# Kernel optimization log

Measured on AMD Instinct MI355X. Metric: run time of the kernel, lower is better.

## Reference

```python
import jax, jax.numpy as jnp
import numpy as np

DIM = 1024
HEADS = 16
DIM_HEAD = 64
INNER = HEADS * DIM_HEAD  # 1024
SCALE = DIM_HEAD ** -0.5


def setup_inputs() -> dict:
    key = jax.random.key(0)
    k1, k2, k3, k4 = jax.random.split(key, 4)
    x = jax.random.normal(k1, (2, 2048, DIM), dtype=jnp.float32)
    # nn.Linear(dim, inner*3, bias=False): weight [3*inner, dim]; store transposed [dim, 3*inner]
    w_qkv = jax.random.normal(k2, (DIM, 3 * INNER), dtype=jnp.float32) * (DIM ** -0.5)
    w_out = jax.random.normal(k3, (INNER, DIM), dtype=jnp.float32) * (INNER ** -0.5)
    b_out = jax.random.normal(k4, (DIM,), dtype=jnp.float32) * 0.02
    return {"x": x, "w_qkv": w_qkv, "w_out": w_out, "b_out": b_out}


def _attention(x, w_qkv, w_out, b_out):
    b, n, _ = x.shape
    qkv = x @ w_qkv  # [b, n, 3*inner]
    q_chunk = qkv[..., :INNER]  # NOTE: source bug — q, k, v all come from chunk 0
    def split_heads(t):
        return t.reshape(b, n, HEADS, DIM_HEAD).transpose(0, 2, 1, 3)  # b h n d
    q = split_heads(q_chunk) * SCALE
    k = split_heads(q_chunk)
    v = split_heads(q_chunk)
    dots = jnp.einsum('bhid,bhjd->bhij', q, k)
    mask_value = -jnp.finfo(dots.dtype).max
    causal_mask = jnp.triu(jnp.ones((n, n), dtype=bool), k=1)
    dots = jnp.where(causal_mask, mask_value, dots)
    attn = jax.nn.softmax(dots, axis=-1)
    out = jnp.einsum('bhij,bhjd->bhid', attn, v)
    out = out.transpose(0, 2, 1, 3).reshape(b, n, INNER)
    return out @ w_out + b_out


def reference(x, w_qkv, w_out, b_out):
    return _attention(x, w_qkv, w_out, b_out)
```

## Files before the change

### kernel.cpp

```cpp
#include <hip/hip_runtime.h>
#include <hip/hip_bf16.h>

typedef __attribute__((ext_vector_type(8))) short short8;
typedef __attribute__((ext_vector_type(4))) short bf16x4;
typedef __attribute__((ext_vector_type(4))) float floatx4;

#define MFMA16(a, b, c) __builtin_amdgcn_mfma_f32_16x16x32_bf16((a), (b), (c), 0, 0, 0)

#if defined(__HIP_DEVICE_COMPILE__)
  #if __has_builtin(__builtin_amdgcn_mfma_f32_16x16x16bf16_1k)
    #define MFMA_PV(a, b, c) __builtin_amdgcn_mfma_f32_16x16x16bf16_1k((a), (b), (c), 0, 0, 0)
  #elif __has_builtin(__builtin_amdgcn_mfma_f32_16x16x16_bf16)
    #define MFMA_PV(a, b, c) __builtin_amdgcn_mfma_f32_16x16x16_bf16((a), (b), (c), 0, 0, 0)
  #else
    #error "no 16x16x16 bf16 MFMA builtin found on device pass"
  #endif
#else
  #define MFMA_PV(a, b, c) (c)
#endif

#define SEQ    2048
#define DIMM   1024
#define HEADS  16
#define DHEAD  64
#define ROWS   4096
#define K1 0.18033688011112043f
#define K2 (-34.62468098133512f)

__global__ void cvt_bf16_kernel(const float* __restrict__ src,
                                __hip_bfloat16* __restrict__ dst) {
    const size_t i = (size_t)(blockIdx.x * 256 + threadIdx.x) * 4;
    floatx4 v = *(const floatx4*)(src + i);
    union { bf16x4 s; __hip_bfloat16 h[4]; } u;
#pragma unroll
    for (int j = 0; j < 4; j++) u.h[j] = __float2bfloat16(v[j]);
    *(bf16x4*)(dst + i) = u.s;
}

__global__ __launch_bounds__(256) void transpose_cvt_kernel(
    const float* __restrict__ W, __hip_bfloat16* __restrict__ WT, int ld) {
    __shared__ __hip_bfloat16 tile[64][72];
    const int tid = threadIdx.x;
    const int r = tid >> 2, c0 = (tid & 3) * 16;
    const int k0 = blockIdx.x * 64;
    const int n0 = blockIdx.y * 64;
    const float* src = W + (size_t)(k0 + r) * ld + n0 + c0;
    union { short8 v; __hip_bfloat16 h[8]; } a0, a1;
#pragma unroll
    for (int j = 0; j < 8; j++) {
        a0.h[j] = __float2bfloat16(src[j]);
        a1.h[j] = __float2bfloat16(src[8 + j]);
    }
    *(short8*)&tile[r][c0]     = a0.v;
    *(short8*)&tile[r][c0 + 8] = a1.v;
    __syncthreads();
    union { short8 v; __hip_bfloat16 h[8]; } u0, u1;
#pragma unroll
    for (int j = 0; j < 8; j++) {
        u0.h[j] = tile[c0 + j][r];
        u1.h[j] = tile[c0 + 8 + j][r];
    }
    __hip_bfloat16* dst = WT + (size_t)(n0 + r) * 1024 + k0 + c0;
    *(short8*)dst       = u0.v;
    *(short8*)(dst + 8) = u1.v;
}

__global__ __launch_bounds__(256) void transpose_t_kernel(
    const __hip_bfloat16* __restrict__ t,
    __hip_bfloat16* __restrict__ Tt) {
    __shared__ __hip_bfloat16 tile[64][72];
    const int tid = threadIdx.x;
    const int r = tid >> 2, c0 = (tid & 3) * 16;
    const int row0 = blockIdx.x * 64;
    const int col0 = blockIdx.y * 64;
    const __hip_bfloat16* src = t + (size_t)(row0 + r) * DIMM + col0 + c0;
    *(short8*)&tile[r][c0]     = *(const short8*)src;
    *(short8*)&tile[r][c0 + 8] = *(const short8*)(src + 8);
    __syncthreads();
    union { short8 v; __hip_bfloat16 h[8]; } u0, u1;
#pragma unroll
    for (int j = 0; j < 8; j++) {
        u0.h[j] = tile[c0 + j][r];
        u1.h[j] = tile[c0 + 8 + j][r];
    }
    __hip_bfloat16* dst = Tt + (size_t)(col0 + r) * ROWS + row0 + c0;
    *(short8*)dst       = u0.v;
    *(short8*)(dst + 8) = u1.v;
}

template <typename CT>
__global__ __launch_bounds__(256) void gemm_bf_kernel(
    const __hip_bfloat16* __restrict__ A,
    const __hip_bfloat16* __restrict__ BT,
    const float* __restrict__ bias,
    CT* __restrict__ C, int M, int N, int K) {
    __shared__ __align__(16) __hip_bfloat16 As[2][64][68];
    __shared__ __align__(16) __hip_bfloat16 Bs[2][64][68];

    const int tid  = threadIdx.x;
    const int lane = tid & 63, wid = tid >> 6;
    const int wm   = wid >> 1, wn = wid & 1;
    const int quad = lane >> 4, l15 = lane & 15;
    const int bm = blockIdx.y * 64, bn = blockIdx.x * 64;

    floatx4 acc[2][2];
#pragma unroll
    for (int r = 0; r < 2; r++)
#pragma unroll
        for (int c = 0; c < 2; c++) acc[r][c] = (floatx4){0.f, 0.f, 0.f, 0.f};

    const int sr = tid >> 2, sc = (tid & 3) * 16;
    short8 ra[2], rb[2];
    auto load_tile = [&](int k0) {
        const __hip_bfloat16* pa = A + (size_t)(bm + sr) * K + k0 + sc;
        ra[0] = *(const short8*)pa; ra[1] = *(const short8*)(pa + 8);
        const __hip_bfloat16* pb = BT + (size_t)(bn + sr) * K + k0 + sc;
        rb[0] = *(const short8*)pb; rb[1] = *(const short8*)(pb + 8);
    };
    auto store_tile = [&](int buf) {
        *(short8*)&As[buf][sr][sc]     = ra[0];
        *(short8*)&As[buf][sr][sc + 8] = ra[1];
        *(short8*)&Bs[buf][sr][sc]     = rb[0];
        *(short8*)&Bs[buf][sr][sc + 8] = rb[1];
    };

    load_tile(0);
    store_tile(0);
    if (K > 64) load_tile(64);
    __syncthreads();

    const int nk = K >> 6;
    for (int kb = 0; kb < nk; ++kb) {
        const int buf = kb & 1;
#pragma unroll
        for (int ks = 0; ks < 2; ks++) {
            short8 af[2], bf[2];
#pragma unroll
            for (int r = 0; r < 2; r++)
                af[r] = *(const short8*)&As[buf][wm * 32 + r * 16 + l15][ks * 32 + quad * 8];
#pragma unroll
            for (int c = 0; c < 2; c++)
                bf[c] = *(const short8*)&Bs[buf][wn * 32 + c * 16 + l15][ks * 32 + quad * 8];
#pragma unroll
            for (int r = 0; r < 2; r++)
#pragma unroll
                for (int c = 0; c < 2; c++)
                    acc[r][c] = MFMA16(af[r], bf[c], acc[r][c]);
        }
        if (kb + 1 < nk) store_tile(buf ^ 1);
        if (kb + 2 < nk) load_tile((kb + 2) << 6);
        __syncthreads();
    }

#pragma unroll
    for (int c = 0; c < 2; c++) {
        const int col = bn + wn * 32 + c * 16 + l15;
        const float bv = bias ? bias[col] : 0.f;
#pragma unroll
        for (int r = 0; r < 2; r++) {
            const int row0 = bm + wm * 32 + r * 16 + quad * 4;
#pragma unroll
            for (int i = 0; i < 4; i++) {
                const float v = acc[r][c][i] + bv;
                if constexpr (__is_same(CT, float))
                    C[(size_t)(row0 + i) * N + col] = v;
                else
                    C[(size_t)(row0 + i) * N + col] = __float2bfloat16(v);
            }
        }
    }
}

template <typename AT, typename CT>
__global__ __launch_bounds__(256) void gemm_fp_kernel(
    const AT* __restrict__ A, const float* __restrict__ B,
    const float* __restrict__ bias, CT* __restrict__ C,
    int M, int N, int K, int ldb) {
    __shared__ __align__(16) __hip_bfloat16 As[2][64][40];
    __shared__ __align__(16) __hip_bfloat16 Bs[2][128][40];
    const int tid = threadIdx.x;
    const int lane = tid & 63, wid = tid >> 6;
    const int wm = wid >> 1, wn = wid & 1;
    const int quad = lane >> 4, l15 = lane & 15;
    const int bm = blockIdx.y * 64, bn = blockIdx.x * 128;
    floatx4 acc[2][4];
#pragma unroll
    for (int r = 0; r < 2; r++)
#pragma unroll
        for (int c = 0; c < 4; c++) acc[r][c] = (floatx4){0.f, 0.f, 0.f, 0.f};
    const int a_lr = tid >> 2, a_lc = (tid & 3) * 8;
    const int b_kr = tid & 31, b_nc = (tid >> 5) * 16;
    floatx4 raf0, raf1; short8 rab; floatx4 rb[4];
    auto load_tile = [&](int k0) {
        const AT* pa = A + (size_t)(bm + a_lr) * K + k0 + a_lc;
        if constexpr (__is_same(AT, float)) {
            raf0 = *(const floatx4*)pa; raf1 = *(const floatx4*)(pa + 4);
        } else { rab = *(const short8*)pa; }
        const float* pb = B + (size_t)(k0 + b_kr) * ldb + bn + b_nc;
#pragma unroll
        for (int q = 0; q < 4; q++) rb[q] = *(const floatx4*)(pb + 4 * q);
    };
    auto store_tile = [&](int buf) {
        if constexpr (__is_same(AT, float)) {
            __align__(16) __hip_bfloat16 hh[8];
#pragma unroll
            for (int j = 0; j < 4; j++) {
                hh[j] = __float2bfloat16(raf0[j]); hh[4 + j] = __float2bfloat16(raf1[j]);
            }
            *(short8*)&As[buf][a_lr][a_lc] = *(short8*)&hh[0];
        } else { *(short8*)&As[buf][a_lr][a_lc] = rab; }
#pragma unroll
        for (int q = 0; q < 4; q++)
#pragma unroll
            for (int j = 0; j < 4; j++)
                Bs[buf][b_nc + 4 * q + j][b_kr] = __float2bfloat16(rb[q][j]);
    };
    load_tile(0); store_tile(0);
    if (K > 32) load_tile(32);
    __syncthreads();
    const int nk = K >> 5;
    for (int kb = 0; kb < nk; ++kb) {
        const int buf = kb & 1;
        short8 af[2], bf[4];
#pragma unroll
        for (int r = 0; r < 2; r++)
            af[r] = *(const short8*)&As[buf][wm * 32 + r * 16 + l15][quad * 8];
#pragma unroll
        for (int c = 0; c < 4; c++)
            bf[c] = *(const short8*)&Bs[buf][wn * 64 + c * 16 + l15][quad * 8];
#pragma unroll
        for (int r = 0; r < 2; r++)
#pragma unroll
            for (int c = 0; c < 4; c++)
                acc[r][c] = MFMA16(af[r], bf[c], acc[r][c]);
        if (kb + 1 < nk) store_tile(buf ^ 1);
        if (kb + 2 < nk) load_tile((kb + 2) << 5);
        __syncthreads();
    }
#pragma unroll
    for (int c = 0; c < 4; c++) {
        const int col = bn + wn * 64 + c * 16 + l15;
        const float bv = bias ? bias[col] : 0.f;
#pragma unroll
        for (int r = 0; r < 2; r++) {
            const int row0 = bm + wm * 32 + r * 16 + quad * 4;
#pragma unroll
            for (int i = 0; i < 4; i++) {
                const float v = acc[r][c][i] + bv;
                if constexpr (__is_same(CT, float)) C[(size_t)(row0 + i) * N + col] = v;
                else C[(size_t)(row0 + i) * N + col] = __float2bfloat16(v);
            }
        }
    }
}

__global__ __launch_bounds__(256) void attn_kernel(
    const __hip_bfloat16* __restrict__ T,
    const __hip_bfloat16* __restrict__ Tt,
    __hip_bfloat16* __restrict__ O) {
    __shared__ __align__(16) __hip_bfloat16 Ks[2][64][68];
    __shared__ __align__(16) __hip_bfloat16 Vt[2][64][68];

    const int tid  = threadIdx.x;
    const int lane = tid & 63, wid = tid >> 6;
    const int quad = lane >> 4, l15 = lane & 15;

    const int bx = blockIdx.x;
    const int half = bx >> 9, idx = bx & 511;
    const int g = idx & 15, h = (idx >> 4) & 15, b = idx >> 8;
    const int qt = half ? g : 31 - g;

    const size_t rowbase = (size_t)b * SEQ;
    const int hoff  = h * DHEAD;
    const int qrow0 = qt * 64;

    short8 qf[2];
    {
        const __hip_bfloat16* qp =
            T + (rowbase + qrow0 + wid * 16 + l15) * DIMM + hoff + quad * 8;
        qf[0] = *(const short8*)qp;
        qf[1] = *(const short8*)(qp + 32);
    }

    float l_lane = 0.f;
    floatx4 accO[4];
#pragma unroll
    for (int dt = 0; dt < 4; dt++) accO[dt] = (floatx4){0.f,0.f,0.f,0.f};

    const int sr = tid >> 2;
    const int sc = (tid & 3) * 16;

    short8 rK0, rK1, rV0, rV1;
    auto load_tile = [&](int kt) {
        const __hip_bfloat16* pK = T + (rowbase + kt * 64 + sr) * DIMM + hoff + sc;
        rK0 = *(const short8*)pK; rK1 = *(const short8*)(pK + 8);
        const __hip_bfloat16* pV =
            Tt + (size_t)(hoff + sr) * ROWS + rowbase + kt * 64 + sc;
        rV0 = *(const short8*)pV; rV1 = *(const short8*)(pV + 8);
    };
    auto store_tile = [&](int buf) {
        *(short8*)&Ks[buf][sr][sc]     = rK0;
        *(short8*)&Ks[buf][sr][sc + 8] = rK1;
        *(short8*)&Vt[buf][sr][sc]     = rV0;
        *(short8*)&Vt[buf][sr][sc + 8] = rV1;
    };

    const int last = qt;
    load_tile(0);
    store_tile(0);
    if (last >= 1) load_tile(1);
    __syncthreads();

    for (int kt = 0; kt <= last; ++kt) {
        const int buf = kt & 1;

        floatx4 s[4];
#pragma unroll
        for (int c = 0; c < 4; c++) {
            s[c] = (floatx4){0.f,0.f,0.f,0.f};
#pragma unroll
            for (int ks = 0; ks < 2; ks++) {
                short8 kfr = *(const short8*)&Ks[buf][c * 16 + l15][ks * 32 + quad * 8];
                s[c] = MFMA16(kfr, qf[ks], s[c]);
            }
        }

        bf16x4 pk[4];
        const bool need_mask = (kt == last);
#pragma unroll
        for (int c = 0; c < 4; c++) {
            union { bf16x4 v; __hip_bfloat16 hh[4]; } u;
            float sum = 0.f;
#pragma unroll
            for (int i = 0; i < 4; i++) {
                float v = exp2f(fmaf(s[c][i], K1, K2));
                if (need_mask) {
                    const int key  = kt * 64 + c * 16 + quad * 4 + i;
                    const int qrow = qrow0 + wid * 16 + l15;
                    if (key > qrow) v = 0.f;
                }
                sum += v;
                u.hh[i] = __float2bfloat16(v);
            }
            l_lane += sum;
            pk[c] = u.v;
        }

#pragma unroll
        for (int c = 0; c < 4; c++)
#pragma unroll
            for (int dt = 0; dt < 4; dt++) {
                bf16x4 vb = *(const bf16x4*)&Vt[buf][dt * 16 + l15][c * 16 + quad * 4];
                accO[dt] = MFMA_PV(pk[c], vb, accO[dt]);
            }

        if (kt < last)      store_tile(buf ^ 1);
        if (kt + 2 <= last) load_tile(kt + 2);
        __syncthreads();
    }

    l_lane += __shfl_xor(l_lane, 16);
    l_lane += __shfl_xor(l_lane, 32);
    float inv[4];
#pragma unroll
    for (int i = 0; i < 4; i++)
        inv[i] = 1.f / __shfl(l_lane, quad * 4 + i, 64);
#pragma unroll
    for (int dt = 0; dt < 4; dt++)
#pragma unroll
        for (int i = 0; i < 4; i++) {
            const size_t row = rowbase + qrow0 + wid * 16 + quad * 4 + i;
            O[row * DIMM + hoff + dt * 16 + l15] =
                __float2bfloat16(accO[dt][i] * inv[i]);
        }
}

extern "C" void kernel_launch(void* const* d_in, const int* in_sizes, int n_in,
                              void* d_out, int out_size, void* d_ws, size_t ws_size,
                              hipStream_t stream) {
    const float* x     = (const float*)d_in[0];
    const float* w_qkv = (const float*)d_in[1];
    const float* w_out = (const float*)d_in[2];
    const float* b_out = (const float*)d_in[3];
    float* out = (float*)d_out;

    __hip_bfloat16* t  = (__hip_bfloat16*)d_out;
    __hip_bfloat16* Tt = (__hip_bfloat16*)((char*)d_out + (8u << 20));
    char* ws = (char*)d_ws;
    __hip_bfloat16* ob = (__hip_bfloat16*)ws;

    if (ws_size >= (size_t)(20u << 20)) {
        __hip_bfloat16* xb  = (__hip_bfloat16*)(ws + (8u  << 20));
        __hip_bfloat16* w1t = (__hip_bfloat16*)(ws + (16u << 20));
        __hip_bfloat16* w2t = (__hip_bfloat16*)(ws + (18u << 20));

        cvt_bf16_kernel<<<4096, 256, 0, stream>>>(x, xb);
        transpose_cvt_kernel<<<dim3(16, 16), 256, 0, stream>>>(w_qkv, w1t, 3 * DIMM);
        transpose_cvt_kernel<<<dim3(16, 16), 256, 0, stream>>>(w_out, w2t, DIMM);

        gemm_bf_kernel<__hip_bfloat16><<<dim3(16, 64), 256, 0, stream>>>(
            xb, w1t, nullptr, t, ROWS, DIMM, DIMM);
        transpose_t_kernel<<<dim3(64, 16), 256, 0, stream>>>(t, Tt);
        attn_kernel<<<dim3(1024), 256, 0, stream>>>(t, Tt, ob);
        gemm_bf_kernel<float><<<dim3(16, 64), 256, 0, stream>>>(
            ob, w2t, b_out, out, ROWS, DIMM, DIMM);
    } else {
        gemm_fp_kernel<float, __hip_bfloat16><<<dim3(8, 64), 256, 0, stream>>>(
            x, w_qkv, nullptr, t, ROWS, DIMM, DIMM, 3 * DIMM);
        transpose_t_kernel<<<dim3(64, 16), 256, 0, stream>>>(t, Tt);
        attn_kernel<<<dim3(1024), 256, 0, stream>>>(t, Tt, ob);
        gemm_fp_kernel<__hip_bfloat16, float><<<dim3(8, 64), 256, 0, stream>>>(
            ob, w_out, b_out, out, ROWS, DIMM, DIMM, DIMM);
    }
}
```

Measured before the change: 167.5 us.

## Use direct global-to-LDS loads with XOR swizzle and 64x128 GEMM tiles

Rewrites the bf16 GEMM's staging so global tiles go straight into LDS via global_load_lds, skipping the register round trip and the separate store phase. The LDS layout becomes an unpadded K=32 tile with an XOR swizzle to avoid bank conflicts. The block tile widens from 64x64 to 64x128 so each wave computes 2x4 MFMA tiles, and launch bounds now request two blocks per CU. The risks are more K iterations (and syncs) per block, half as many blocks in the grid, and correctness depending on how global_load_lds places each lane's 16 bytes in LDS.

```diff
diff --git a/kernel.cpp b/kernel.cpp
--- a/kernel.cpp
+++ b/kernel.cpp
@@ -18,6 +18,13 @@
 #else
   #define MFMA_PV(a, b, c) (c)
 #endif
+
+__device__ __forceinline__ void gload16(const void* g, void* l) {
+    __builtin_amdgcn_global_load_lds(
+        (const __attribute__((address_space(1))) unsigned int*)g,
+        (__attribute__((address_space(3))) unsigned int*)l,
+        16, 0, 0);
+}
 
 #define SEQ    2048
 #define DIMM   1024
@@ -89,72 +96,77 @@
 }
 
 template <typename CT>
-__global__ __launch_bounds__(256) void gemm_bf_kernel(
+__global__ __launch_bounds__(256, 2) void gemm_bf_kernel(
     const __hip_bfloat16* __restrict__ A,
     const __hip_bfloat16* __restrict__ BT,
     const float* __restrict__ bias,
     CT* __restrict__ C, int M, int N, int K) {
-    __shared__ __align__(16) __hip_bfloat16 As[2][64][68];
-    __shared__ __align__(16) __hip_bfloat16 Bs[2][64][68];
+    __shared__ __align__(16) __hip_bfloat16 As[2][64 * 32];
+    __shared__ __align__(16) __hip_bfloat16 Bs[2][128 * 32];
 
     const int tid  = threadIdx.x;
     const int lane = tid & 63, wid = tid >> 6;
     const int wm   = wid >> 1, wn = wid & 1;
     const int quad = lane >> 4, l15 = lane & 15;
-    const int bm = blockIdx.y * 64, bn = blockIdx.x * 64;
-
-    floatx4 acc[2][2];
+    const int bm = blockIdx.y * 64, bn = blockIdx.x * 128;
+
+    floatx4 acc[2][4];
 #pragma unroll
     for (int r = 0; r < 2; r++)
 #pragma unroll
-        for (int c = 0; c < 2; c++) acc[r][c] = (floatx4){0.f, 0.f, 0.f, 0.f};
-
-    const int sr = tid >> 2, sc = (tid & 3) * 16;
-    short8 ra[2], rb[2];
-    auto load_tile = [&](int k0) {
-        const __hip_bfloat16* pa = A + (size_t)(bm + sr) * K + k0 + sc;
-        ra[0] = *(const short8*)pa; ra[1] = *(const short8*)(pa + 8);
-        const __hip_bfloat16* pb = BT + (size_t)(bn + sr) * K + k0 + sc;
-        rb[0] = *(const short8*)pb; rb[1] = *(const short8*)(pb + 8);
-    };
-    auto store_tile = [&](int buf) {
-        *(short8*)&As[buf][sr][sc]     = ra[0];
-        *(short8*)&As[buf][sr][sc + 8] = ra[1];
-        *(short8*)&Bs[buf][sr][sc]     = rb[0];
-        *(short8*)&Bs[buf][sr][sc + 8] = rb[1];
-    };
-
-    load_tile(0);
-    store_tile(0);
-    if (K > 64) load_tile(64);
+        for (int c = 0; c < 4; c++) acc[r][c] = (floatx4){0.f, 0.f, 0.f, 0.f};
+
+    const int a_r = tid >> 2;
+    const int a_c = (tid & 3) ^ ((a_r >> 1) & 3);
+    auto issueA = [&](int k0, int buf) {
+        gload16(A + (size_t)(bm + a_r) * K + k0 + a_c * 8,
+                (char*)&As[buf][0] + wid * 1024);
+    };
+    auto issueB = [&](int k0, int buf) {
+#pragma unroll
+        for (int j = 0; j < 2; j++) {
+            const int s = j * 256 + tid;
+            const int r = s >> 2;
+            const int c = (s & 3) ^ ((r >> 1) & 3);
+            gload16(BT + (size_t)(bn + r) * K + k0 + c * 8,
+                    (char*)&Bs[buf][0] + j * 4096 + wid * 1024);
+        }
+    };
+
+    issueA(0, 0); issueB(0, 0);
     __syncthreads();
 
-    const int nk = K >> 6;
+    const int nk = K >> 5;
     for (int kb = 0; kb < nk; ++kb) {
         const int buf = kb & 1;
-#pragma unroll
-        for (int ks = 0; ks < 2; ks++) {
-            short8 af[2], bf[2];
-#pragma unroll
-            for (int r = 0; r < 2; r++)
-                af[r] = *(const short8*)&As[buf][wm * 32 + r * 16 + l15][ks * 32 + quad * 8];
-#pragma unroll
-            for (int c = 0; c < 2; c++)
-                bf[c] = *(const short8*)&Bs[buf][wn * 32 + c * 16 + l15][ks * 32 + quad * 8];
-#pragma unroll
-            for (int r = 0; r < 2; r++)
-#pragma unroll
-                for (int c = 0; c < 2; c++)
-                    acc[r][c] = MFMA16(af[r], bf[c], acc[r][c]);
-        }
-        if (kb + 1 < nk) store_tile(buf ^ 1);
-        if (kb + 2 < nk) load_tile((kb + 2) << 6);
+        if (kb + 1 < nk) {
+            issueA((kb + 1) << 5, buf ^ 1);
+            issueB((kb + 1) << 5, buf ^ 1);
+        }
+        short8 af[2], bf[4];
+#pragma unroll
+        for (int r = 0; r < 2; r++) {
+            const int row = wm * 32 + r * 16 + l15;
+            af[r] = *(const short8*)((const char*)&As[buf][0] + row * 64 +
+                                     ((quad ^ ((row >> 1) & 3)) << 4));
+        }
+#pragma unroll
+        for (int c = 0; c < 4; c++) {
+            const int row = wn * 64 + c * 16 + l15;
+            bf[c] = *(const short8*)((const char*)&Bs[buf][0] + row * 64 +
+                                     ((quad ^ ((row >> 1) & 3)) << 4));
+        }
+#pragma unroll
+        for (int r = 0; r < 2; r++)
+#pragma unroll
+            for (int c = 0; c < 4; c++)
+                acc[r][c] = MFMA16(af[r], bf[c], acc[r][c]);
         __syncthreads();
     }
 
 #pragma unroll
-    for (int c = 0; c < 2; c++) {
-        const int col = bn + wn * 32 + c * 16 + l15;
+    for (int c = 0; c < 4; c++) {
+        const int col = bn + wn * 64 + c * 16 + l15;
         const float bv = bias ? bias[col] : 0.f;
 #pragma unroll
         for (int r = 0; r < 2; r++) {
@@ -398,11 +410,11 @@
         transpose_cvt_kernel<<<dim3(16, 16), 256, 0, stream>>>(w_qkv, w1t, 3 * DIMM);
         transpose_cvt_kernel<<<dim3(16, 16), 256, 0, stream>>>(w_out, w2t, DIMM);
 
-        gemm_bf_kernel<__hip_bfloat16><<<dim3(16, 64), 256, 0, stream>>>(
+        gemm_bf_kernel<__hip_bfloat16><<<dim3(8, 64), 256, 0, stream>>>(
             xb, w1t, nullptr, t, ROWS, DIMM, DIMM);
         transpose_t_kernel<<<dim3(64, 16), 256, 0, stream>>>(t, Tt);
         attn_kernel<<<dim3(1024), 256, 0, stream>>>(t, Tt, ob);
-        gemm_bf_kernel<float><<<dim3(16, 64), 256, 0, stream>>>(
+        gemm_bf_kernel<float><<<dim3(8, 64), 256, 0, stream>>>(
             ob, w2t, b_out, out, ROWS, DIMM, DIMM);
     } else {
         gemm_fp_kernel<float, __hip_bfloat16><<<dim3(8, 64), 256, 0, stream>>>(
```

Result: slower. 171.7 us (+2.6%).
